# Optimization experiments

Hardware: AMD Instinct MI355X
Metric: run time of the kernel (lower is better)

Reference implementation:

```python
import jax, jax.numpy as jnp
import numpy as np

CR = 64                      # cond_repeat
DILS = tuple(2 ** i for _ in range(2) for i in range(10))  # 2 blocks x 10 layers
Q_ZERO = 128


def setup_inputs() -> dict:
    key = jax.random.key(0)
    B, C, TE = 8, 64, 8          # batch, cond channels, encoding timesteps
    R, S, Q = 128, 128, 256      # residual, skip, classes
    L = len(DILS)
    ks = jax.random.split(key, 12)
    sc = 0.1
    return {
        "encodings": jax.random.normal(ks[0], (B, C, TE), jnp.float32),
        "first_w": jax.random.normal(ks[1], (R, 1, 2), jnp.float32) * sc,
        "first_b": jnp.zeros((R,), jnp.float32),
        "causal_w": jax.random.normal(ks[2], (L, 2 * R, R, 2), jnp.float32) * sc,
        "causal_b": jnp.zeros((L, 2 * R), jnp.float32),
        "cond_w": jax.random.normal(ks[3], (L, 2 * R, C), jnp.float32) * sc,
        "cond_b": jnp.zeros((L, 2 * R), jnp.float32),
        "res_w": jax.random.normal(ks[4], (L, R, R), jnp.float32) * sc,
        "res_b": jnp.zeros((L, R), jnp.float32),
        "skip_w": jax.random.normal(ks[5], (L, S, R), jnp.float32) * sc,
        "skip_b": jnp.zeros((L, S), jnp.float32),
        "skipc_w": jax.random.normal(ks[6], (S, R), jnp.float32) * sc,
        "skipc_b": jnp.zeros((S,), jnp.float32),
        "fc_w": jax.random.normal(ks[7], (S, S), jnp.float32) * sc,
        "fc_b": jnp.zeros((S,), jnp.float32),
        "condf_w": jax.random.normal(ks[8], (S, C), jnp.float32) * sc,
        "condf_b": jnp.zeros((S,), jnp.float32),
        "logits_w": jax.random.normal(ks[9], (Q, S), jnp.float32) * sc,
        "logits_b": jnp.zeros((Q,), jnp.float32),
    }


def _generate(encodings, first_w, first_b, causal_w, causal_b, cond_w, cond_b,
              res_w, res_b, skip_w, skip_b, skipc_w, skipc_b, fc_w, fc_b,
              condf_w, condf_b, logits_w, logits_b):
    B = encodings.shape[0]
    R = res_w.shape[1]
    T = encodings.shape[2] * CR

    # ring buffers emulate QueuedConv1d (queue length = dilation, zero-initialized)
    buf_first0 = jnp.zeros((B, 1), jnp.float32)
    bufs0 = tuple(jnp.zeros((B, d, R), jnp.float32) for d in DILS)
    sample0 = jnp.full((B,), Q_ZERO, jnp.int32)

    def step(carry, t):
        sample, buf_first, bufs = carry
        x = sample.astype(jnp.float32) / 255.0 - 0.5                      # [B]
        c = jax.lax.dynamic_index_in_dim(encodings, t // CR, axis=2,
                                         keepdims=False)                  # [B,C]
        # first causal conv (1 -> R, kernel 2): tap0 on delayed sample, tap1 on current
        prev0 = buf_first[:, 0]
        buf_first = buf_first.at[:, 0].set(x)
        res = (prev0[:, None] * first_w[None, :, 0, 0]
               + x[:, None] * first_w[None, :, 0, 1] + first_b)           # [B,R]
        skip = res @ skipc_w.T + skipc_b                                  # [B,S]
        new_bufs = []
        for l, d in enumerate(DILS):
            idx = jnp.mod(t, d)
            prev = jax.lax.dynamic_index_in_dim(bufs[l], idx, axis=1, keepdims=False)
            new_bufs.append(jax.lax.dynamic_update_index_in_dim(bufs[l], res, idx, axis=1))
            z = (prev @ causal_w[l, :, :, 0].T + res @ causal_w[l, :, :, 1].T
                 + causal_b[l] + c @ cond_w[l].T + cond_b[l])             # [B,2R]
            gate, out = jnp.split(z, 2, axis=1)
            h = jax.nn.sigmoid(gate) * jnp.tanh(out)                      # [B,R]
            res = res + h @ res_w[l].T + res_b[l]
            skip = skip + h @ skip_w[l].T + skip_b[l]
        s = jax.nn.relu(skip) @ fc_w.T + fc_b + c @ condf_w.T + condf_b
        logits = jax.nn.relu(s) @ logits_w.T + logits_b                   # [B,Q]
        sample = jnp.argmax(logits, axis=1).astype(jnp.int32)             # 'max' sampling
        return (sample, buf_first, tuple(new_bufs)), (sample, logits)

    _, (samples, logits) = jax.lax.scan(step, (sample0, buf_first0, bufs0),
                                        jnp.arange(T))
    return samples, logits  # [T,B] int32, [T,B,Q] float32


def reference(encodings, first_w, first_b, causal_w, causal_b, cond_w, cond_b,
              res_w, res_b, skip_w, skip_b, skipc_w, skipc_b, fc_w, fc_b,
              condf_w, condf_b, logits_w, logits_b):
    return _generate(encodings, first_w, first_b, causal_w, causal_b, cond_w, cond_b,
                     res_w, res_b, skip_w, skip_b, skipc_w, skipc_b, fc_w, fc_b,
                     condf_w, condf_b, logits_w, logits_b)
```

## Files before the change

kernel.cpp:

```cpp
#include <hip/hip_runtime.h>
#include <math.h>

#define BB 8
#define TT 512
#define LL 20
#define NBLK 64
#define NTHR 256

typedef float f4 __attribute__((ext_vector_type(4)));
typedef unsigned long long ull;

__constant__ int c_dil[LL] = {1,2,4,8,16,32,64,128,256,512,
                              1,2,4,8,16,32,64,128,256,512};
__constant__ int c_roff2[LL] = {-1,0,4096,10240,20480,38912,73728,141312,274432,538624,
                                1064960,1068032,1072128,1078272,1088512,1106944,
                                1141760,1209344,1342464,1606656};

constexpr size_t OFF_RING = 0;
constexpr size_t OFF_X    = 2132992;
constexpr size_t OFF_CHK  = 2145280;
constexpr size_t OFF_CB2  = 4766720;

#define P_WSKIPC 0
#define P_WFC    256
#define P_WLOG   512
#define P_WF0    1024
#define P_WF1    1152
#define P_FB     1280
#define P_CONDZ  1408
#define P_SFC    2048
#define P_RESB   2064
#define P_SKIPB  2104
#define P_LOGB   2144
#define P_SKIPCB 2148
#define P_XCUR   2152
#define P_XPREV  2160
#define P_XNEW   2168
#define P_SZ     2176
#define P_SL     2208
#define P_SKACC  2240
#define P_R2     2256
#define P_WS     2272
#define P_CF     2292
#define P_PREVF  2820
#define P_HF     4932
#define P_RESF   7044
#define P_RES0   8100
#define P_CAND   10212
#define POOL_FL  11300

__device__ __forceinline__ f4 ldx(const f4* p) {
    f4 r;
    asm volatile("global_load_dwordx4 %0, %1, off sc0 sc1\n\ts_waitcnt vmcnt(0)"
                 : "=v"(r) : "v"(p) : "memory");
    return r;
}
__device__ __forceinline__ void ldx2(const f4* p0, const f4* p1, f4& a, f4& b) {
    asm volatile("global_load_dwordx4 %0, %2, off sc0 sc1\n\t"
                 "global_load_dwordx4 %1, %3, off sc0 sc1\n\t"
                 "s_waitcnt vmcnt(0)"
                 : "=v"(a), "=v"(b) : "v"(p0), "v"(p1) : "memory");
}
__device__ __forceinline__ void ldx4v(const f4* p0, const f4* p1, const f4* p2, const f4* p3,
                                      f4& a, f4& b, f4& c, f4& d) {
    asm volatile("global_load_dwordx4 %0, %4, off sc0 sc1\n\t"
                 "global_load_dwordx4 %1, %5, off sc0 sc1\n\t"
                 "global_load_dwordx4 %2, %6, off sc0 sc1\n\t"
                 "global_load_dwordx4 %3, %7, off sc0 sc1\n\t"
                 "s_waitcnt vmcnt(0)"
                 : "=v"(a),"=v"(b),"=v"(c),"=v"(d)
                 : "v"(p0),"v"(p1),"v"(p2),"v"(p3) : "memory");
}
__device__ __forceinline__ void stx_nd(f4* p, f4 v) {
    asm volatile("global_store_dwordx4 %0, %1, off sc0 sc1"
                 :: "v"(p), "v"(v) : "memory");
}

__device__ __forceinline__ float dot4(f4 a, f4 b) {
    return a.x*b.x + a.y*b.y + a.z*b.z + a.w*b.w;
}

__device__ __forceinline__ void publish16(f4* slot, int J, const float* sl, int e) {
    if (threadIdx.x < 6) {
        int q = threadIdx.x;
        f4 v;
        v.x = sl[3*q];
        v.y = (3*q+1 < 16) ? sl[3*q+1] : 0.f;
        v.z = (3*q+2 < 16) ? sl[3*q+2] : 0.f;
        v.w = __int_as_float(e);
        stx_nd(slot + J*6 + q, v);
    }
}
__device__ __forceinline__ void scat16(float* dst, f4 v, int vi, bool dorelu) {
    int j = vi / 6, q = vi - 6*j;
    #pragma unroll
    for (int i = 0; i < 3; ++i) {
        int E = 3*q + i;
        if (E < 16) {
            float x = v[i];
            if (dorelu) x = fmaxf(x, 0.f);
            dst[(E & 7)*132 + 2*j + (E >> 3)] = x;
        }
    }
}
__device__ __forceinline__ void consume16(const f4* slot, int e, float* dst, bool dorelu) {
    int m = threadIdx.x;
    const f4 *p0 = slot + m, *p1 = slot + 256 + m;
    f4 a, b;
    bool two = (m < 128);
    if (two) ldx2(p0, p1, a, b); else a = ldx(p0);
    while (__float_as_int(a.w) != e) { __builtin_amdgcn_s_sleep(1); a = ldx(p0); }
    if (two) { while (__float_as_int(b.w) != e) { __builtin_amdgcn_s_sleep(1); b = ldx(p1); } }
    scat16(dst, a, m, dorelu);
    if (two) scat16(dst, b, m + 256, dorelu);
}
__device__ __forceinline__ void consume_dual(const f4* sa, int ea, float* da,
                                             const f4* sb, int eb, float* db) {
    int m = threadIdx.x;
    const f4 *pa0 = sa + m, *pa1 = sa + 256 + m;
    const f4 *pb0 = sb + m, *pb1 = sb + 256 + m;
    f4 a0, a1, b0, b1;
    bool two = (m < 128);
    if (two) ldx4v(pa0, pa1, pb0, pb1, a0, a1, b0, b1);
    else     ldx2(pa0, pb0, a0, b0);
    while (__float_as_int(a0.w) != ea) { __builtin_amdgcn_s_sleep(1); a0 = ldx(pa0); }
    if (two) { while (__float_as_int(a1.w) != ea) { __builtin_amdgcn_s_sleep(1); a1 = ldx(pa1); } }
    while (__float_as_int(b0.w) != eb) { __builtin_amdgcn_s_sleep(1); b0 = ldx(pb0); }
    if (two) { while (__float_as_int(b1.w) != eb) { __builtin_amdgcn_s_sleep(1); b1 = ldx(pb1); } }
    scat16(da, a0, m, false);
    scat16(db, b0, m, false);
    if (two) { scat16(da, a1, m + 256, false); scat16(db, b1, m + 256, false); }
}
__device__ __forceinline__ void consume16c(const f4* slot, int e, float* dst) {
    int m = threadIdx.x;
    const f4 *p0 = slot + m, *p1 = slot + 256 + m;
    f4 a, b;
    bool two = (m < 128);
    if (two) ldx2(p0, p1, a, b); else a = ldx(p0);
    while (__float_as_int(a.w) != e) { __builtin_amdgcn_s_sleep(1); a = ldx(p0); }
    if (two) { while (__float_as_int(b.w) != e) { __builtin_amdgcn_s_sleep(1); b = ldx(p1); } }
    #pragma unroll
    for (int s = 0; s < 2; ++s) {
        if (s == 1 && !two) break;
        f4 v = s ? b : a;
        int vi = m + s*256;
        int jb = vi / 6, q = vi - 6*jb;
        #pragma unroll
        for (int i = 0; i < 3; ++i) {
            int E = 3*q + i;
            if (E < 16) dst[(E >> 3)*544 + (E & 7)*68 + jb] = v[i];
        }
    }
}

__global__ void wn_pack(const float* __restrict__ causal_w,
                        const float* __restrict__ res_w,
                        const float* __restrict__ skip_w,
                        const float* __restrict__ causal_b,
                        const float* __restrict__ cond_b,
                        const float* __restrict__ res_b,
                        f4* __restrict__ chk, float* __restrict__ cb2)
{
    int bx = blockIdx.x;
    int J = bx / 20, l = bx - J*20;
    int tid = threadIdx.x;
    for (int s = 0; s < 2; ++s) {
        int p = tid + s*256;
        f4 v; v.x = 0.f; v.y = 0.f; v.z = 0.f; v.w = 0.f;
        if (p < 384) {
            int i = p >> 5, gk = p & 31, g = gk >> 3, k = gk & 7;
            int row = (g < 2) ? (2*J + g) : (128 + 2*J + (g - 2));
            int c0 = 16*k + 4*(i & 3);
            if (i < 8) {
                int tap = i >> 2;
                const float* src = causal_w + ((size_t)(l*256 + row)*128 + c0)*2 + tap;
                v.x = src[0]; v.y = src[2]; v.z = src[4]; v.w = src[6];
            } else if (l >= 1) {
                float a0=0.f, a1=0.f, a2=0.f, a3=0.f;
                const float* w1 = causal_w + ((size_t)(l*256 + row)*128)*2 + 1;
                const float* rw = res_w + (size_t)(l-1)*128*128 + c0;
                for (int m2 = 0; m2 < 128; ++m2) {
                    float wv = w1[2*m2];
                    const float* rr = rw + (size_t)m2*128;
                    a0 += wv*rr[0]; a1 += wv*rr[1]; a2 += wv*rr[2]; a3 += wv*rr[3];
                }
                v.x = a0; v.y = a1; v.z = a2; v.w = a3;
            }
        } else {
            int q = p - 384, u = q >> 5, wk = q & 31, w = wk >> 3, k = wk & 7;
            int r = w & 1, isSkip = w >> 1;
            const float* mm = (isSkip ? skip_w : res_w)
                              + ((size_t)(l*128 + 2*J + r)*128 + 16*k + 4*u);
            v.x = mm[0]; v.y = mm[1]; v.z = mm[2]; v.w = mm[3];
        }
        chk[(size_t)(J*20 + l)*512 + p] = v;
    }
    if (tid < 4) {
        int row = (tid < 2) ? (2*J + tid) : (128 + 2*J + (tid - 2));
        float zb = 0.f;
        if (l >= 1) {
            const float* w1 = causal_w + ((size_t)(l*256 + row)*128)*2 + 1;
            for (int m2 = 0; m2 < 128; ++m2) zb += w1[2*m2]*res_b[(l-1)*128 + m2];
        }
        cb2[l*256 + row] = causal_b[l*256 + row] + cond_b[l*256 + row] + zb;
    }
}

__global__ __launch_bounds__(NTHR, 1) void wn_gen(
    const float* __restrict__ enc,
    const float* __restrict__ first_w,  const float* __restrict__ first_b,
    const float* __restrict__ cond_w,
    const float* __restrict__ res_b,    const float* __restrict__ skip_b,
    const float* __restrict__ skipc_w,  const float* __restrict__ skipc_b,
    const float* __restrict__ fc_w,     const float* __restrict__ fc_b,
    const float* __restrict__ condf_w,  const float* __restrict__ condf_b,
    const float* __restrict__ logits_w, const float* __restrict__ logits_b,
    float* __restrict__ wsf, float* __restrict__ out)
{
    extern __shared__ float pool[];
    const int tid = threadIdx.x;
    const int J = blockIdx.x;
    float* ring = wsf + OFF_RING;
    f4* xb = (f4*)(wsf + OFF_X);
    const f4* chk = (const f4*)(wsf + OFF_CHK);
    const float* cb2 = wsf + OFF_CB2;
    int* wsl = (int*)(pool + P_WS);

    if (tid < 256) {
        int r = tid >> 7, i = tid & 127;
        pool[P_WSKIPC + tid] = skipc_w[(size_t)(2*J + r)*128 + i];
        pool[P_WFC + tid]    = fc_w[(size_t)(2*J + r)*128 + i];
    }
    for (int m = tid; m < 512; m += NTHR) {
        int w = m >> 7, i = m & 127;
        pool[P_WLOG + m] = logits_w[(size_t)(4*J + w)*128 + i];
    }
    if (tid < 128) {
        pool[P_WF0 + tid] = first_w[2*tid];
        pool[P_WF1 + tid] = first_w[2*tid + 1];
        pool[P_FB + tid]  = first_b[tid];
    }
    if (tid < 40) {
        int l = tid >> 1, r = tid & 1;
        pool[P_RESB + tid]  = res_b[l*128 + 2*J + r];
        pool[P_SKIPB + tid] = skip_b[l*128 + 2*J + r];
    }
    if (tid < 4) pool[P_LOGB + tid] = logits_b[4*J + tid];
    if (tid < 2) pool[P_SKIPCB + tid] = skipc_b[2*J + tid];
    for (int m = tid; m < 2112; m += NTHR) pool[P_RES0 + m] = 0.f;
    if (tid < 8) { pool[P_XCUR + tid] = 128.f/255.f - 0.5f; pool[P_XPREV + tid] = 0.f; }
    __syncthreads();

    const int zi = (tid >> 6)*8 + (tid & 7);

    f4 cw[16], nw[16];
    {
        const f4* cp = chk + (size_t)(J*20)*512;
        #pragma unroll
        for (int i = 0; i < 12; ++i) cw[i] = cp[i*32 + zi];
        #pragma unroll
        for (int u = 0; u < 4; ++u) cw[12+u] = cp[384 + u*32 + zi];
    }

    ull pfa = 0, pfb = 0;
    float zpre = 0.f;
    int e = 0, er_pending = 0;

    for (int t = 0; t < TT; ++t) {
        if ((t & 63) == 0) {
            int te = t >> 6;
            for (int m = tid; m < 512; m += NTHR) {
                int b = m >> 6, j = m & 63;
                pool[P_CF + b*66 + j] = enc[(size_t)b*512 + j*8 + te];
            }
            __syncthreads();
            for (int m = tid; m < 640; m += NTHR) {
                int l = m >> 5, rem = m & 31, g = rem >> 3, b = rem & 7;
                int grow = (g < 2) ? (2*J + g) : (128 + 2*J + (g - 2));
                float acc = cb2[l*256 + grow];
                const float* cwp = cond_w + (size_t)(l*256 + grow)*64;
                const float* cf = pool + P_CF + b*66;
                for (int j = 0; j < 64; ++j) acc += cwp[j]*cf[j];
                pool[P_CONDZ + l*32 + g*8 + b] = acc;
            }
            if (tid < 16) {
                int r = tid >> 3, b = tid & 7, row = 2*J + r;
                float acc = fc_b[row] + condf_b[row];
                const float* cwp = condf_w + (size_t)row*64;
                const float* cf = pool + P_CF + b*66;
                for (int j = 0; j < 64; ++j) acc += cwp[j]*cf[j];
                pool[P_SFC + r*8 + b] = acc;
            }
            __syncthreads();
        }

        if (tid < 19) {
            int L = tid + 1, D = c_dil[L] + 2;
            int w = wsl[tid];
            wsl[tid] = (t == 0) ? 0 : ((w + 1 >= D) ? 0 : w + 1);
        }
        const int cur = t & 1;
        for (int m = tid; m < 1024; m += NTHR) {
            int b = m >> 7, r = m & 127;
            pool[P_RES0 + cur*1056 + b*132 + r] =
                pool[P_XPREV + b]*pool[P_WF0 + r] + pool[P_XCUR + b]*pool[P_WF1 + r] + pool[P_FB + r];
        }
        __syncthreads();
        {
            int w = tid >> 6, lane = tid & 63, b = lane >> 3, k = lane & 7;
            if (w < 2) {
                const float* wr = pool + P_WSKIPC + w*128 + 16*k;
                const float* rs = pool + P_RES0 + cur*1056 + b*132 + 16*k;
                float acc = 0.f;
                #pragma unroll
                for (int u = 0; u < 4; ++u)
                    acc += dot4(*(const f4*)(wr + 4*u), *(const f4*)(rs + 4*u));
                acc += __shfl_xor(acc,1); acc += __shfl_xor(acc,2); acc += __shfl_xor(acc,4);
                if (k == 0) pool[P_SKACC + w*8 + b] = acc + pool[P_SKIPCB + w];
            }
        }
        if (tid < 16) {
            int r = tid >> 3, b = tid & 7;
            pool[P_R2 + r*8 + b] = pool[P_RES0 + cur*1056 + b*132 + 2*J + r];
        }

        for (int l = 0; l < LL; ++l) {
            if (l <= 18) {
                int b = tid >> 5, c = (tid & 31)*4;
                union { ull u; float f[2]; } u0, u1;
                u0.u = pfa; u1.u = pfb;
                float* dp = pool + P_PREVF + ((l+1)&1)*1056 + b*132 + c;
                dp[0] = u0.f[0]; dp[1] = u0.f[1]; dp[2] = u1.f[0]; dp[3] = u1.f[1];
            }
            {
                int ln = (l + 1) % 20;
                const f4* cp = chk + (size_t)(J*20 + ln)*512;
                #pragma unroll
                for (int i = 0; i < 12; ++i) nw[i] = cp[i*32 + zi];
                #pragma unroll
                for (int u = 0; u < 4; ++u) nw[12+u] = cp[384 + u*32 + zi];
            }
            if (l <= 17) {
                int L = l + 2, d = c_dil[L];
                if (t >= d) {
                    int D = d + 2;
                    int rsl = wsl[L-1] + 2; if (rsl >= D) rsl -= D;
                    const float* rp = ring + c_roff2[L] + (size_t)rsl*1024 + tid*4;
                    pfa = __hip_atomic_load((const ull*)rp,     __ATOMIC_RELAXED, __HIP_MEMORY_SCOPE_AGENT);
                    pfb = __hip_atomic_load((const ull*)(rp+2), __ATOMIC_RELAXED, __HIP_MEMORY_SCOPE_AGENT);
                } else { pfa = 0; pfb = 0; }
            }
            {
                int g = tid >> 6, lane = tid & 63, b = lane >> 3, k = lane & 7;
                (void)g;
                const float* rs = ((l <= 1) ? pool + P_RES0 + cur*1056 : pool + P_RESF)
                                  + b*132 + 16*k;
                float acc;
                if (l == 0) {
                    const float* pv = pool + P_RES0 + (cur^1)*1056 + b*132 + 16*k;
                    acc = 0.f;
                    #pragma unroll
                    for (int u = 0; u < 4; ++u) acc += dot4(cw[u], *(const f4*)(pv + 4*u));
                } else acc = zpre;
                #pragma unroll
                for (int u = 0; u < 4; ++u) acc += dot4(cw[4+u], *(const f4*)(rs + 4*u));
                if (l >= 1) {
                    const float* hh = pool + P_HF + ((l-1)&1)*1056 + b*132 + 16*k;
                    #pragma unroll
                    for (int u = 0; u < 4; ++u) acc += dot4(cw[8+u], *(const f4*)(hh + 4*u));
                }
                acc += __shfl_xor(acc,1); acc += __shfl_xor(acc,2); acc += __shfl_xor(acc,4);
                if (k == 0) pool[P_SZ + (tid>>6)*8 + b] = acc;
            }
            __syncthreads();

            ++e; int eh = e;
            if (tid < 64) {
                if (tid < 16) {
                    int r = tid & 1, b = tid >> 1;
                    float gg = pool[P_SZ + r*8 + b]     + pool[P_CONDZ + l*32 + r*8 + b];
                    float oo = pool[P_SZ + (2+r)*8 + b] + pool[P_CONDZ + l*32 + (2+r)*8 + b];
                    pool[P_SL + r*8 + b] = (1.f/(1.f + expf(-gg))) * tanhf(oo);
                }
                publish16(xb + (size_t)(eh & 3)*768, J, pool + P_SL, eh);
            }
            if (l <= 18) {
                int lane = tid & 63, b = lane >> 3, k = lane & 7;
                const float* pv = pool + P_PREVF + ((l+1)&1)*1056 + b*132 + 16*k;
                float z = 0.f;
                #pragma unroll
                for (int u = 0; u < 4; ++u) z += dot4(nw[u], *(const f4*)(pv + 4*u));
                zpre = z;
            }
            if (l == 0 || l == 19)
                consume16(xb + (size_t)(eh & 3)*768, eh, pool + P_HF + (l&1)*1056, false);
            else
                consume_dual(xb + (size_t)(eh & 3)*768, eh, pool + P_HF + (l&1)*1056,
                             xb + (size_t)(er_pending & 3)*768, er_pending, pool + P_RESF);
            __syncthreads();

            {
                int w = tid >> 6, lane = tid & 63, b = lane >> 3, k = lane & 7;
                int r = w & 1, isSkip = w >> 1;
                if (isSkip || l <= 18) {
                    const float* hh = pool + P_HF + (l&1)*1056 + b*132 + 16*k;
                    float acc = 0.f;
                    #pragma unroll
                    for (int u = 0; u < 4; ++u) acc += dot4(cw[12+u], *(const f4*)(hh + 4*u));
                    acc += __shfl_xor(acc,1); acc += __shfl_xor(acc,2); acc += __shfl_xor(acc,4);
                    if (k == 0) {
                        if (isSkip) {
                            pool[P_SKACC + r*8 + b] += acc + pool[P_SKIPB + l*2 + r];
                        } else {
                            float v = pool[P_R2 + r*8 + b] + acc + pool[P_RESB + l*2 + r];
                            pool[P_R2 + r*8 + b] = v;
                            pool[P_SL + r*8 + b] = v;
                            int ws2 = wsl[l];
                            float* wp = ring + c_roff2[l+1] + (size_t)ws2*1024 + b*128 + 2*J + r;
                            __hip_atomic_store(wp, v, __ATOMIC_RELAXED, __HIP_MEMORY_SCOPE_AGENT);
                        }
                    }
                }
            }
            __syncthreads();
            if (l <= 17) {
                ++e;
                if (tid < 64) publish16(xb + (size_t)(e & 3)*768, J, pool + P_SL, e);
                er_pending = e;
            }
            #pragma unroll
            for (int i = 0; i < 16; ++i) cw[i] = nw[i];
        }

        {
            int d = c_dil[1];
            if (t + 1 >= d) {
                int D = d + 2;
                int rsl = wsl[0] + 3; while (rsl >= D) rsl -= D;
                const float* rp = ring + c_roff2[1] + (size_t)rsl*1024 + tid*4;
                pfa = __hip_atomic_load((const ull*)rp,     __ATOMIC_RELAXED, __HIP_MEMORY_SCOPE_AGENT);
                pfb = __hip_atomic_load((const ull*)(rp+2), __ATOMIC_RELAXED, __HIP_MEMORY_SCOPE_AGENT);
            } else { pfa = 0; pfb = 0; }
        }
        ++e;
        publish16(xb + (size_t)(e & 3)*768, J, pool + P_SKACC, e);
        consume16(xb + (size_t)(e & 3)*768, e, pool + P_HF, false);
        __syncthreads();
        {
            int w = tid >> 6, lane = tid & 63, b = lane >> 3, k = lane & 7;
            if (w < 2) {
                const float* wr = pool + P_WFC + w*128 + 16*k;
                const float* sk = pool + P_HF + b*132 + 16*k;
                float acc = 0.f;
                #pragma unroll
                for (int u = 0; u < 4; ++u) {
                    f4 sv = *(const f4*)(sk + 4*u);
                    sv.x = fmaxf(sv.x, 0.f); sv.y = fmaxf(sv.y, 0.f);
                    sv.z = fmaxf(sv.z, 0.f); sv.w = fmaxf(sv.w, 0.f);
                    acc += dot4(*(const f4*)(wr + 4*u), sv);
                }
                acc += __shfl_xor(acc,1); acc += __shfl_xor(acc,2); acc += __shfl_xor(acc,4);
                if (k == 0) pool[P_SL + w*8 + b] = acc + pool[P_SFC + w*8 + b];
            }
        }
        __syncthreads();
        ++e;
        publish16(xb + (size_t)(e & 3)*768, J, pool + P_SL, e);
        consume16(xb + (size_t)(e & 3)*768, e, pool + P_RESF, true);
        __syncthreads();
        {
            int g = tid >> 6, lane = tid & 63, b = lane >> 3, k = lane & 7;
            const float* wr = pool + P_WLOG + g*128 + 16*k;
            const float* sv = pool + P_RESF + b*132 + 16*k;
            float acc = 0.f;
            #pragma unroll
            for (int u = 0; u < 4; ++u) acc += dot4(*(const f4*)(wr + 4*u), *(const f4*)(sv + 4*u));
            acc += __shfl_xor(acc,1); acc += __shfl_xor(acc,2); acc += __shfl_xor(acc,4);
            if (k == 0) {
                float v = acc + pool[P_LOGB + g];
                pool[P_SZ + g*8 + b] = v;
                out[4096 + ((size_t)(t*BB + b))*256 + 4*J + g] = v;
            }
        }
        __syncthreads();
        if (tid < 8) {
            int b = tid;
            float best = -3.4e38f; int bi = 0;
            #pragma unroll
            for (int g = 0; g < 4; ++g) {
                float v = pool[P_SZ + g*8 + b];
                if (v > best) { best = v; bi = 4*J + g; }
            }
            pool[P_SL + b] = best;
            pool[P_SL + 8 + b] = (float)bi;
        }
        ++e;
        if (tid < 64) publish16(xb + (size_t)(e & 3)*768, J, pool + P_SL, e);
        consume16c(xb + (size_t)(e & 3)*768, e, pool + P_CAND);
        __syncthreads();
        {
            int b = tid >> 5, j = tid & 31;
            float v0 = pool[P_CAND + b*68 + j],       v1 = pool[P_CAND + b*68 + j + 32];
            int   i0 = (int)pool[P_CAND + 544 + b*68 + j];
            int   i1 = (int)pool[P_CAND + 544 + b*68 + j + 32];
            float bv; int bib;
            if (v1 > v0 || (v1 == v0 && i1 < i0)) { bv = v1; bib = i1; }
            else                                  { bv = v0; bib = i0; }
            #pragma unroll
            for (int m = 16; m >= 1; m >>= 1) {
                float ov = __shfl_xor(bv, m);
                int   oi = __shfl_xor(bib, m);
                if (ov > bv || (ov == bv && oi < bib)) { bv = ov; bib = oi; }
            }
            if (j == 0) {
                pool[P_XNEW + b] = (float)bib;
                if (J == 0) out[t*BB + b] = (float)bib;
            }
        }
        __syncthreads();
        if (tid < 8) {
            pool[P_XPREV + tid] = pool[P_XCUR + tid];
            pool[P_XCUR + tid]  = pool[P_XNEW + tid]*(1.f/255.f) - 0.5f;
        }
        __syncthreads();
    }
}

extern "C" void kernel_launch(void* const* d_in, const int* in_sizes, int n_in,
                              void* d_out, int out_size, void* d_ws, size_t ws_size,
                              hipStream_t stream) {
    const float* enc      = (const float*)d_in[0];
    const float* first_w  = (const float*)d_in[1];
    const float* first_b  = (const float*)d_in[2];
    const float* causal_w = (const float*)d_in[3];
    const float* causal_b = (const float*)d_in[4];
    const float* cond_w   = (const float*)d_in[5];
    const float* cond_b   = (const float*)d_in[6];
    const float* res_w    = (const float*)d_in[7];
    const float* res_b    = (const float*)d_in[8];
    const float* skip_w   = (const float*)d_in[9];
    const float* skip_b   = (const float*)d_in[10];
    const float* skipc_w  = (const float*)d_in[11];
    const float* skipc_b  = (const float*)d_in[12];
    const float* fc_w     = (const float*)d_in[13];
    const float* fc_b     = (const float*)d_in[14];
    const float* condf_w  = (const float*)d_in[15];
    const float* condf_b  = (const float*)d_in[16];
    const float* logits_w = (const float*)d_in[17];
    const float* logits_b = (const float*)d_in[18];

    float* wsf = (float*)d_ws;
    float* out = (float*)d_out;

    wn_pack<<<NBLK*LL, NTHR, 0, stream>>>(causal_w, res_w, skip_w,
                                          causal_b, cond_b, res_b,
                                          (f4*)(wsf + OFF_CHK), wsf + OFF_CB2);
    wn_gen<<<NBLK, NTHR, 98304, stream>>>(
        enc, first_w, first_b, cond_w, res_b, skip_b, skipc_w, skipc_b,
        fc_w, fc_b, condf_w, condf_b, logits_w, logits_b, wsf, out);
}
```

Measured before the change: 39.40 ms.

## Compute full fc layer redundantly per block to drop a grid exchange round

Result: faster. 38.52 ms (-2.2%).

```diff
diff --git a/kernel.cpp b/kernel.cpp
--- a/kernel.cpp
+++ b/kernel.cpp
@@ -19,16 +19,14 @@
 constexpr size_t OFF_RING = 0;
 constexpr size_t OFF_X    = 2132992;
 constexpr size_t OFF_CHK  = 2145280;
-constexpr size_t OFF_CB2  = 4766720;
+constexpr size_t OFF_CB2  = 5094400;
 
 #define P_WSKIPC 0
-#define P_WFC    256
 #define P_WLOG   512
 #define P_WF0    1024
 #define P_WF1    1152
 #define P_FB     1280
 #define P_CONDZ  1408
-#define P_SFC    2048
 #define P_RESB   2064
 #define P_SKIPB  2104
 #define P_LOGB   2144
@@ -47,7 +45,8 @@
 #define P_RESF   7044
 #define P_RES0   8100
 #define P_CAND   10212
-#define POOL_FL  11300
+#define P_SFC2   11300
+#define POOL_FL  12324
 
 __device__ __forceinline__ f4 ldx(const f4* p) {
     f4 r;
@@ -108,9 +107,16 @@
     const f4 *p0 = slot + m, *p1 = slot + 256 + m;
     f4 a, b;
     bool two = (m < 128);
-    if (two) ldx2(p0, p1, a, b); else a = ldx(p0);
-    while (__float_as_int(a.w) != e) { __builtin_amdgcn_s_sleep(1); a = ldx(p0); }
-    if (two) { while (__float_as_int(b.w) != e) { __builtin_amdgcn_s_sleep(1); b = ldx(p1); } }
+    if (two) {
+        ldx2(p0, p1, a, b);
+        while (__float_as_int(a.w) != e || __float_as_int(b.w) != e) {
+            __builtin_amdgcn_s_sleep(1);
+            ldx2(p0, p1, a, b);
+        }
+    } else {
+        a = ldx(p0);
+        while (__float_as_int(a.w) != e) { __builtin_amdgcn_s_sleep(1); a = ldx(p0); }
+    }
     scat16(dst, a, m, dorelu);
     if (two) scat16(dst, b, m + 256, dorelu);
 }
@@ -121,12 +127,20 @@
     const f4 *pb0 = sb + m, *pb1 = sb + 256 + m;
     f4 a0, a1, b0, b1;
     bool two = (m < 128);
-    if (two) ldx4v(pa0, pa1, pb0, pb1, a0, a1, b0, b1);
-    else     ldx2(pa0, pb0, a0, b0);
-    while (__float_as_int(a0.w) != ea) { __builtin_amdgcn_s_sleep(1); a0 = ldx(pa0); }
-    if (two) { while (__float_as_int(a1.w) != ea) { __builtin_amdgcn_s_sleep(1); a1 = ldx(pa1); } }
-    while (__float_as_int(b0.w) != eb) { __builtin_amdgcn_s_sleep(1); b0 = ldx(pb0); }
-    if (two) { while (__float_as_int(b1.w) != eb) { __builtin_amdgcn_s_sleep(1); b1 = ldx(pb1); } }
+    if (two) {
+        ldx4v(pa0, pa1, pb0, pb1, a0, a1, b0, b1);
+        while (__float_as_int(a0.w) != ea || __float_as_int(a1.w) != ea ||
+               __float_as_int(b0.w) != eb || __float_as_int(b1.w) != eb) {
+            __builtin_amdgcn_s_sleep(1);
+            ldx4v(pa0, pa1, pb0, pb1, a0, a1, b0, b1);
+        }
+    } else {
+        ldx2(pa0, pb0, a0, b0);
+        while (__float_as_int(a0.w) != ea || __float_as_int(b0.w) != eb) {
+            __builtin_amdgcn_s_sleep(1);
+            ldx2(pa0, pb0, a0, b0);
+        }
+    }
     scat16(da, a0, m, false);
     scat16(db, b0, m, false);
     if (two) { scat16(da, a1, m + 256, false); scat16(db, b1, m + 256, false); }
@@ -136,9 +150,16 @@
     const f4 *p0 = slot + m, *p1 = slot + 256 + m;
     f4 a, b;
     bool two = (m < 128);
-    if (two) ldx2(p0, p1, a, b); else a = ldx(p0);
-    while (__float_as_int(a.w) != e) { __builtin_amdgcn_s_sleep(1); a = ldx(p0); }
-    if (two) { while (__float_as_int(b.w) != e) { __builtin_amdgcn_s_sleep(1); b = ldx(p1); } }
+    if (two) {
+        ldx2(p0, p1, a, b);
+        while (__float_as_int(a.w) != e || __float_as_int(b.w) != e) {
+            __builtin_amdgcn_s_sleep(1);
+            ldx2(p0, p1, a, b);
+        }
+    } else {
+        a = ldx(p0);
+        while (__float_as_int(a.w) != e) { __builtin_amdgcn_s_sleep(1); a = ldx(p0); }
+    }
     #pragma unroll
     for (int s = 0; s < 2; ++s) {
         if (s == 1 && !two) break;
@@ -164,8 +185,9 @@
     int bx = blockIdx.x;
     int J = bx / 20, l = bx - J*20;
     int tid = threadIdx.x;
-    for (int s = 0; s < 2; ++s) {
+    for (int s = 0; s < 3; ++s) {
         int p = tid + s*256;
+        if (p >= 576) break;
         f4 v; v.x = 0.f; v.y = 0.f; v.z = 0.f; v.w = 0.f;
         if (p < 384) {
             int i = p >> 5, gk = p & 31, g = gk >> 3, k = gk & 7;
@@ -186,14 +208,19 @@
                 }
                 v.x = a0; v.y = a1; v.z = a2; v.w = a3;
             }
-        } else {
+        } else if (p < 512) {
             int q = p - 384, u = q >> 5, wk = q & 31, w = wk >> 3, k = wk & 7;
             int r = w & 1, isSkip = w >> 1;
             const float* mm = (isSkip ? skip_w : res_w)
                               + ((size_t)(l*128 + 2*J + r)*128 + 16*k + 4*u);
             v.x = mm[0]; v.y = mm[1]; v.z = mm[2]; v.w = mm[3];
-        }
-        chk[(size_t)(J*20 + l)*512 + p] = v;
+        } else {
+            int q = p - 512, vv = q >> 3, low3 = q & 7;
+            int r = low3 >> 2, k2 = low3 & 3;
+            const float* mm = res_w + ((size_t)(l*128 + 2*J + r)*128 + 32*k2 + 4*vv);
+            v.x = mm[0]; v.y = mm[1]; v.z = mm[2]; v.w = mm[3];
+        }
+        chk[(size_t)(J*20 + l)*576 + p] = v;
     }
     if (tid < 4) {
         int row = (tid < 2) ? (2*J + tid) : (128 + 2*J + (tid - 2));
@@ -229,7 +256,6 @@
     if (tid < 256) {
         int r = tid >> 7, i = tid & 127;
         pool[P_WSKIPC + tid] = skipc_w[(size_t)(2*J + r)*128 + i];
-        pool[P_WFC + tid]    = fc_w[(size_t)(2*J + r)*128 + i];
     }
     for (int m = tid; m < 512; m += NTHR) {
         int w = m >> 7, i = m & 127;
@@ -252,14 +278,27 @@
     __syncthreads();
 
     const int zi = (tid >> 6)*8 + (tid & 7);
-
-    f4 cw[16], nw[16];
+    const int low3 = (tid & 63) & 7;
+
+    f4 fcw2[16];
     {
-        const f4* cp = chk + (size_t)(J*20)*512;
+        int og = tid >> 3, k = tid & 7;
+        #pragma unroll
+        for (int oi = 0; oi < 4; ++oi)
+            #pragma unroll
+            for (int u = 0; u < 4; ++u)
+                fcw2[oi*4+u] = *(const f4*)(fc_w + (size_t)(og*4+oi)*128 + 16*k + 4*u);
+    }
+
+    f4 cw[16], nw[16], cw2[8], nw2[8];
+    {
+        const f4* cp = chk + (size_t)(J*20)*576;
         #pragma unroll
         for (int i = 0; i < 12; ++i) cw[i] = cp[i*32 + zi];
         #pragma unroll
         for (int u = 0; u < 4; ++u) cw[12+u] = cp[384 + u*32 + zi];
+        #pragma unroll
+        for (int v = 0; v < 8; ++v) cw2[v] = cp[512 + v*8 + low3];
     }
 
     ull pfa = 0, pfb = 0;
@@ -283,13 +322,13 @@
                 for (int j = 0; j < 64; ++j) acc += cwp[j]*cf[j];
                 pool[P_CONDZ + l*32 + g*8 + b] = acc;
             }
-            if (tid < 16) {
-                int r = tid >> 3, b = tid & 7, row = 2*J + r;
-                float acc = fc_b[row] + condf_b[row];
-                const float* cwp = condf_w + (size_t)row*64;
+            for (int m = tid; m < 1024; m += NTHR) {
+                int o = m >> 3, b = m & 7;
+                float acc = fc_b[o] + condf_b[o];
+                const float* cwp = condf_w + (size_t)o*64;
                 const float* cf = pool + P_CF + b*66;
                 for (int j = 0; j < 64; ++j) acc += cwp[j]*cf[j];
-                pool[P_SFC + r*8 + b] = acc;
+                pool[P_SFC2 + m] = acc;
             }
             __syncthreads();
         }
@@ -334,11 +373,13 @@
             }
             {
                 int ln = (l + 1) % 20;
-                const f4* cp = chk + (size_t)(J*20 + ln)*512;
+                const f4* cp = chk + (size_t)(J*20 + ln)*576;
                 #pragma unroll
                 for (int i = 0; i < 12; ++i) nw[i] = cp[i*32 + zi];
                 #pragma unroll
                 for (int u = 0; u < 4; ++u) nw[12+u] = cp[384 + u*32 + zi];
+                #pragma unroll
+                for (int v = 0; v < 8; ++v) nw2[v] = cp[512 + v*8 + low3];
             }
             if (l <= 17) {
                 int L = l + 2, d = c_dil[L];
@@ -351,8 +392,7 @@
                 } else { pfa = 0; pfb = 0; }
             }
             {
-                int g = tid >> 6, lane = tid & 63, b = lane >> 3, k = lane & 7;
-                (void)g;
+                int lane = tid & 63, b = lane >> 3, k = lane & 7;
                 const float* rs = ((l <= 1) ? pool + P_RES0 + cur*1056 : pool + P_RESF)
                                   + b*132 + 16*k;
                 float acc;
@@ -400,38 +440,48 @@
             __syncthreads();
 
             {
-                int w = tid >> 6, lane = tid & 63, b = lane >> 3, k = lane & 7;
-                int r = w & 1, isSkip = w >> 1;
-                if (isSkip || l <= 18) {
+                int w = tid >> 6;
+                if (w == 0) {
+                    if (l <= 18) {
+                        int lane = tid & 63, b = lane >> 3;
+                        int r = low3 >> 2, k2 = low3 & 3;
+                        const float* hh = pool + P_HF + (l&1)*1056 + b*132 + 32*k2;
+                        float acc = 0.f;
+                        #pragma unroll
+                        for (int v = 0; v < 8; ++v) acc += dot4(cw2[v], *(const f4*)(hh + 4*v));
+                        acc += __shfl_xor(acc,1); acc += __shfl_xor(acc,2);
+                        if (k2 == 0) {
+                            float vv = pool[P_R2 + r*8 + b] + acc + pool[P_RESB + l*2 + r];
+                            pool[P_R2 + r*8 + b] = vv;
+                            pool[P_SL + r*8 + b] = vv;
+                            int ws2 = wsl[l];
+                            float* wp = ring + c_roff2[l+1] + (size_t)ws2*1024 + b*128 + 2*J + r;
+                            __hip_atomic_store(wp, vv, __ATOMIC_RELAXED, __HIP_MEMORY_SCOPE_AGENT);
+                        }
+                    }
+                } else if (w >= 2) {
+                    int lane = tid & 63, b = lane >> 3, k = lane & 7;
+                    int r = w & 1;
                     const float* hh = pool + P_HF + (l&1)*1056 + b*132 + 16*k;
                     float acc = 0.f;
                     #pragma unroll
                     for (int u = 0; u < 4; ++u) acc += dot4(cw[12+u], *(const f4*)(hh + 4*u));
                     acc += __shfl_xor(acc,1); acc += __shfl_xor(acc,2); acc += __shfl_xor(acc,4);
-                    if (k == 0) {
-                        if (isSkip) {
-                            pool[P_SKACC + r*8 + b] += acc + pool[P_SKIPB + l*2 + r];
-                        } else {
-                            float v = pool[P_R2 + r*8 + b] + acc + pool[P_RESB + l*2 + r];
-                            pool[P_R2 + r*8 + b] = v;
-                            pool[P_SL + r*8 + b] = v;
-                            int ws2 = wsl[l];
-                            float* wp = ring + c_roff2[l+1] + (size_t)ws2*1024 + b*128 + 2*J + r;
-                            __hip_atomic_store(wp, v, __ATOMIC_RELAXED, __HIP_MEMORY_SCOPE_AGENT);
-                        }
-                    }
+                    if (k == 0) pool[P_SKACC + r*8 + b] += acc + pool[P_SKIPB + l*2 + r];
                 }
             }
-            __syncthreads();
             if (l <= 17) {
                 ++e;
-                if (tid < 64) publish16(xb + (size_t)(e & 3)*768, J, pool + P_SL, e);
+                publish16(xb + (size_t)(e & 3)*768, J, pool + P_SL, e);
                 er_pending = e;
             }
             #pragma unroll
             for (int i = 0; i < 16; ++i) cw[i] = nw[i];
-        }
-
+            #pragma unroll
+            for (int v = 0; v < 8; ++v) cw2[v] = nw2[v];
+        }
+
+        __syncthreads();
         {
             int d = c_dil[1];
             if (t + 1 >= d) {
@@ -444,29 +494,38 @@
         }
         ++e;
         publish16(xb + (size_t)(e & 3)*768, J, pool + P_SKACC, e);
-        consume16(xb + (size_t)(e & 3)*768, e, pool + P_HF, false);
+        consume16(xb + (size_t)(e & 3)*768, e, pool + P_HF, true);
         __syncthreads();
         {
-            int w = tid >> 6, lane = tid & 63, b = lane >> 3, k = lane & 7;
-            if (w < 2) {
-                const float* wr = pool + P_WFC + w*128 + 16*k;
-                const float* sk = pool + P_HF + b*132 + 16*k;
-                float acc = 0.f;
-                #pragma unroll
-                for (int u = 0; u < 4; ++u) {
-                    f4 sv = *(const f4*)(sk + 4*u);
-                    sv.x = fmaxf(sv.x, 0.f); sv.y = fmaxf(sv.y, 0.f);
-                    sv.z = fmaxf(sv.z, 0.f); sv.w = fmaxf(sv.w, 0.f);
-                    acc += dot4(*(const f4*)(wr + 4*u), sv);
+            int og = tid >> 3, k = tid & 7;
+            float accs[32];
+            #pragma unroll
+            for (int b = 0; b < 8; ++b) {
+                const float* hh = pool + P_HF + b*132 + 16*k;
+                f4 h0 = *(const f4*)(hh),     h1 = *(const f4*)(hh + 4);
+                f4 h2 = *(const f4*)(hh + 8), h3 = *(const f4*)(hh + 12);
+                #pragma unroll
+                for (int oi = 0; oi < 4; ++oi)
+                    accs[oi*8+b] = dot4(fcw2[oi*4+0], h0) + dot4(fcw2[oi*4+1], h1)
+                                 + dot4(fcw2[oi*4+2], h2) + dot4(fcw2[oi*4+3], h3);
+            }
+            #pragma unroll
+            for (int i = 0; i < 32; ++i) {
+                accs[i] += __shfl_xor(accs[i], 1);
+                accs[i] += __shfl_xor(accs[i], 2);
+                accs[i] += __shfl_xor(accs[i], 4);
+            }
+            if (k == 0) {
+                #pragma unroll
+                for (int oi = 0; oi < 4; ++oi) {
+                    int o = og*4 + oi;
+                    #pragma unroll
+                    for (int b = 0; b < 8; ++b)
+                        pool[P_RESF + b*132 + o] =
+                            fmaxf(accs[oi*8+b] + pool[P_SFC2 + o*8 + b], 0.f);
                 }
-                acc += __shfl_xor(acc,1); acc += __shfl_xor(acc,2); acc += __shfl_xor(acc,4);
-                if (k == 0) pool[P_SL + w*8 + b] = acc + pool[P_SFC + w*8 + b];
-            }
-        }
-        __syncthreads();
-        ++e;
-        publish16(xb + (size_t)(e & 3)*768, J, pool + P_SL, e);
-        consume16(xb + (size_t)(e & 3)*768, e, pool + P_RESF, true);
+            }
+        }
         __syncthreads();
         {
             int g = tid >> 6, lane = tid & 63, b = lane >> 3, k = lane & 7;
```
